# Performance work log

Measured on AMD Instinct MI355X. Metric: run time of the kernel, lower is better.

## Reference

```python
import jax, jax.numpy as jnp
import numpy as np

N_NODES = 100000
N_EDGES = 3200000
K_OPS = 6
D_FEAT = 64


def setup_inputs() -> dict:
    key = jax.random.key(0)
    k1, k2, k3, k4, k5 = jax.random.split(key, 5)
    h_ops = jax.random.normal(k1, (K_OPS, N_NODES, D_FEAT), dtype=jnp.float32)
    weights = jax.random.normal(k2, (K_OPS,), dtype=jnp.float32)  # mixed signs -> exercises w>0 skip
    vals = jax.random.uniform(k3, (N_EDGES,), dtype=jnp.float32)
    row = jnp.sort(jax.random.randint(k4, (N_EDGES,), 0, N_NODES, dtype=jnp.int32))
    col = jax.random.randint(k5, (N_EDGES,), 0, N_NODES, dtype=jnp.int32)
    return {"h_ops": h_ops, "weights": weights, "vals": vals, "row": row, "col": col}


def _spmm(row, col, vals, x, n):
    # sparse (n x n) COO @ dense (n x d): gather source rows, scale, scatter-add to dest rows
    msg = x[col] * vals[:, None]                                  # [E, d]
    return jax.ops.segment_sum(msg, row, num_segments=n, indices_are_sorted=True)


def reference(h_ops, weights, vals, row, col):
    # sum_k: (w_k * spmm(A, H_k)) if w_k > 0 else w_k (scalar broadcast)
    # spmm is linear, so positive-weight branch folds into one spmm of the weighted sum.
    n = h_ops.shape[1]
    pos = weights > 0
    w_pos = jnp.where(pos, weights, 0.0)                          # [K]
    combined = jnp.einsum("k,knd->nd", w_pos, h_ops)              # [N, d]
    out = _spmm(row, col, vals, combined, n)                      # [N, d]
    scalar_term = jnp.sum(jnp.where(pos, 0.0, weights))           # sum of skipped weights
    return out + scalar_term
```

## Files before the change

kernel.cpp:

```cpp
#include <hip/hip_runtime.h>

#define D_FEAT 64
#define MAX_K 8

__device__ __forceinline__ unsigned short f2bf_rne(float f) {
    unsigned int u = __float_as_uint(f);
    u += 0x7FFFu + ((u >> 16) & 1u);
    return (unsigned short)(u >> 16);
}

__device__ __forceinline__ float bf_lo(unsigned int d) { return __uint_as_float(d << 16); }
__device__ __forceinline__ float bf_hi(unsigned int d) { return __uint_as_float(d & 0xffff0000u); }

__global__ __launch_bounds__(256) void combine_bf16_kernel(
    const float* __restrict__ h_ops,
    const float* __restrict__ weights,
    unsigned short* __restrict__ combined,
    int total4, int K) {
    float w[MAX_K];
    for (int k = 0; k < K; ++k) {
        float wk = weights[k];
        w[k] = wk > 0.f ? wk : 0.f;
    }
    int stride = gridDim.x * blockDim.x;
    for (int i = blockIdx.x * blockDim.x + threadIdx.x; i < total4; i += stride) {
        float4 acc = make_float4(0.f, 0.f, 0.f, 0.f);
        for (int k = 0; k < K; ++k) {
            float4 v = reinterpret_cast<const float4*>(h_ops)[(size_t)k * total4 + i];
            acc.x = fmaf(w[k], v.x, acc.x);
            acc.y = fmaf(w[k], v.y, acc.y);
            acc.z = fmaf(w[k], v.z, acc.z);
            acc.w = fmaf(w[k], v.w, acc.w);
        }
        ushort4 o;
        o.x = f2bf_rne(acc.x); o.y = f2bf_rne(acc.y);
        o.z = f2bf_rne(acc.z); o.w = f2bf_rne(acc.w);
        reinterpret_cast<ushort4*>(combined)[i] = o;
    }
}

__global__ __launch_bounds__(256) void build_rowptr_kernel(
    const int* __restrict__ row, int* __restrict__ row_ptr, int E, int N) {
    int stride = gridDim.x * blockDim.x;
    for (int e = blockIdx.x * blockDim.x + threadIdx.x; e < E; e += stride) {
        int r = row[e];
        int rp = (e == 0) ? -1 : row[e - 1];
        for (int x = rp + 1; x <= r; ++x) row_ptr[x] = e;
        if (e == E - 1) {
            for (int x = r + 1; x <= N; ++x) row_ptr[x] = E;
        }
    }
}

__global__ __launch_bounds__(256) void spmm_bf16_w8_kernel(
    const unsigned short* __restrict__ combined,
    const float* __restrict__ vals,
    const int* __restrict__ row_ptr,
    const int* __restrict__ col,
    const float* __restrict__ weights,
    float* __restrict__ out,
    int n_nodes, int K) {
    int wid = (blockIdx.x * blockDim.x + threadIdx.x) >> 6;
    int lane = threadIdx.x & 63;
    if (wid >= n_nodes) return;

    float s = 0.f;
    for (int k = 0; k < K; ++k) {
        float wk = weights[k];
        if (!(wk > 0.f)) s += wk;
    }

    int start = row_ptr[wid];
    int end   = row_ptr[wid + 1];

    int sub = lane >> 3;
    int fl  = lane & 7;

    float a0 = 0.f, a1 = 0.f, a2 = 0.f, a3 = 0.f;
    float a4 = 0.f, a5 = 0.f, a6 = 0.f, a7 = 0.f;

    const uint4* cb = reinterpret_cast<const uint4*>(combined);

    for (int base = start; base < end; base += 16) {
        int iA = base + sub;
        int iB = base + 8 + sub;
        bool okA = iA < end;
        bool okB = iB < end;
        int iAc = okA ? iA : end - 1;
        int iBc = okB ? iB : end - 1;
        int cA = col[iAc];
        int cB = col[iBc];
        float vA = vals[iAc];
        float vB = vals[iBc];
        if (!okA) vA = 0.f;
        if (!okB) vB = 0.f;
        uint4 gA = cb[((size_t)cA << 3) + fl];
        uint4 gB = cb[((size_t)cB << 3) + fl];
        a0 = fmaf(vA, bf_lo(gA.x), a0); a1 = fmaf(vA, bf_hi(gA.x), a1);
        a2 = fmaf(vA, bf_lo(gA.y), a2); a3 = fmaf(vA, bf_hi(gA.y), a3);
        a4 = fmaf(vA, bf_lo(gA.z), a4); a5 = fmaf(vA, bf_hi(gA.z), a5);
        a6 = fmaf(vA, bf_lo(gA.w), a6); a7 = fmaf(vA, bf_hi(gA.w), a7);
        a0 = fmaf(vB, bf_lo(gB.x), a0); a1 = fmaf(vB, bf_hi(gB.x), a1);
        a2 = fmaf(vB, bf_lo(gB.y), a2); a3 = fmaf(vB, bf_hi(gB.y), a3);
        a4 = fmaf(vB, bf_lo(gB.z), a4); a5 = fmaf(vB, bf_hi(gB.z), a5);
        a6 = fmaf(vB, bf_lo(gB.w), a6); a7 = fmaf(vB, bf_hi(gB.w), a7);
    }

#pragma unroll
    for (int m = 8; m <= 32; m <<= 1) {
        a0 += __shfl_xor(a0, m, 64);
        a1 += __shfl_xor(a1, m, 64);
        a2 += __shfl_xor(a2, m, 64);
        a3 += __shfl_xor(a3, m, 64);
        a4 += __shfl_xor(a4, m, 64);
        a5 += __shfl_xor(a5, m, 64);
        a6 += __shfl_xor(a6, m, 64);
        a7 += __shfl_xor(a7, m, 64);
    }

    if (sub == 0) {
        float4* po = reinterpret_cast<float4*>(out + (size_t)wid * D_FEAT + fl * 8);
        po[0] = make_float4(a0 + s, a1 + s, a2 + s, a3 + s);
        po[1] = make_float4(a4 + s, a5 + s, a6 + s, a7 + s);
    }
}

__global__ __launch_bounds__(256) void combine_kernel(
    const float* __restrict__ h_ops,
    const float* __restrict__ weights,
    float* __restrict__ combined,
    int total4, int K) {
    float w[MAX_K];
    for (int k = 0; k < K; ++k) {
        float wk = weights[k];
        w[k] = wk > 0.f ? wk : 0.f;
    }
    int stride = gridDim.x * blockDim.x;
    for (int i = blockIdx.x * blockDim.x + threadIdx.x; i < total4; i += stride) {
        float4 acc = make_float4(0.f, 0.f, 0.f, 0.f);
        for (int k = 0; k < K; ++k) {
            float4 v = reinterpret_cast<const float4*>(h_ops)[(size_t)k * total4 + i];
            acc.x = fmaf(w[k], v.x, acc.x);
            acc.y = fmaf(w[k], v.y, acc.y);
            acc.z = fmaf(w[k], v.z, acc.z);
            acc.w = fmaf(w[k], v.w, acc.w);
        }
        reinterpret_cast<float4*>(combined)[i] = acc;
    }
}

__global__ __launch_bounds__(256) void spmm_kernel_bs(
    const float* __restrict__ combined,
    const float* __restrict__ vals,
    const int* __restrict__ row,
    const int* __restrict__ col,
    const float* __restrict__ weights,
    float* __restrict__ out,
    int n_nodes, int n_edges, int K) {
    int wid = (blockIdx.x * blockDim.x + threadIdx.x) >> 6;
    int lane = threadIdx.x & 63;
    if (wid >= n_nodes) return;

    int lo = 0, hi = n_edges;
    while (lo < hi) { int mid = (lo + hi) >> 1; if (row[mid] < wid) lo = mid + 1; else hi = mid; }
    int start = lo;
    hi = n_edges;
    while (lo < hi) { int mid = (lo + hi) >> 1; if (row[mid] <= wid) lo = mid + 1; else hi = mid; }
    int end = lo;

    float acc = 0.f;
    for (int e = start; e < end; ++e) {
        acc = fmaf(vals[e], combined[(size_t)col[e] * D_FEAT + lane], acc);
    }
    float s = 0.f;
    for (int k = 0; k < K; ++k) {
        float wk = weights[k];
        if (!(wk > 0.f)) s += wk;
    }
    out[(size_t)wid * D_FEAT + lane] = acc + s;
}

__global__ __launch_bounds__(256) void spmm_fused_kernel(
    const float* __restrict__ h_ops,
    const float* __restrict__ vals,
    const int* __restrict__ row,
    const int* __restrict__ col,
    const float* __restrict__ weights,
    float* __restrict__ out,
    int n_nodes, int n_edges, int K, size_t plane) {
    int wid = (blockIdx.x * blockDim.x + threadIdx.x) >> 6;
    int lane = threadIdx.x & 63;
    if (wid >= n_nodes) return;

    float w[MAX_K];
    for (int k = 0; k < K; ++k) {
        float wk = weights[k];
        w[k] = wk > 0.f ? wk : 0.f;
    }
    int lo = 0, hi = n_edges;
    while (lo < hi) { int mid = (lo + hi) >> 1; if (row[mid] < wid) lo = mid + 1; else hi = mid; }
    int start = lo;
    hi = n_edges;
    while (lo < hi) { int mid = (lo + hi) >> 1; if (row[mid] <= wid) lo = mid + 1; else hi = mid; }
    int end = lo;

    float acc = 0.f;
    for (int e = start; e < end; ++e) {
        int c = col[e];
        float v = vals[e];
        float comb = 0.f;
        for (int k = 0; k < K; ++k) {
            comb = fmaf(w[k], h_ops[(size_t)k * plane + (size_t)c * D_FEAT + lane], comb);
        }
        acc = fmaf(v, comb, acc);
    }
    float s = 0.f;
    for (int k = 0; k < K; ++k) {
        float wk = weights[k];
        if (!(wk > 0.f)) s += wk;
    }
    out[(size_t)wid * D_FEAT + lane] = acc + s;
}

extern "C" void kernel_launch(void* const* d_in, const int* in_sizes, int n_in,
                              void* d_out, int out_size, void* d_ws, size_t ws_size,
                              hipStream_t stream) {
    const float* h_ops   = (const float*)d_in[0];
    const float* weights = (const float*)d_in[1];
    const float* vals    = (const float*)d_in[2];
    const int*   row     = (const int*)d_in[3];
    const int*   col     = (const int*)d_in[4];
    float* out = (float*)d_out;

    int K = in_sizes[1];
    if (K > MAX_K) K = MAX_K;
    int E = in_sizes[2];
    int N = out_size / D_FEAT;
    int total = N * D_FEAT;
    size_t need_bf      = (size_t)total * sizeof(unsigned short);
    size_t need_rowptr  = (size_t)(N + 1) * sizeof(int);
    size_t need_f32     = (size_t)total * sizeof(float);

    int spmm_blocks = (N * 64 + 255) / 256;

    if (ws_size >= need_bf + need_rowptr) {
        unsigned short* combined = (unsigned short*)d_ws;
        int* row_ptr = (int*)((char*)d_ws + need_bf);
        int total4 = total / 4;
        combine_bf16_kernel<<<2048, 256, 0, stream>>>(h_ops, weights, combined, total4, K);
        build_rowptr_kernel<<<2048, 256, 0, stream>>>(row, row_ptr, E, N);
        spmm_bf16_w8_kernel<<<spmm_blocks, 256, 0, stream>>>(combined, vals, row_ptr, col,
                                                             weights, out, N, K);
    } else if (ws_size >= need_f32) {
        float* combined = (float*)d_ws;
        int total4 = total / 4;
        combine_kernel<<<2048, 256, 0, stream>>>(h_ops, weights, combined, total4, K);
        spmm_kernel_bs<<<spmm_blocks, 256, 0, stream>>>(combined, vals, row, col,
                                                        weights, out, N, E, K);
    } else {
        spmm_fused_kernel<<<spmm_blocks, 256, 0, stream>>>(h_ops, vals, row, col, weights,
                                                           out, N, E, K, (size_t)total);
    }
}
```

Before: 91.77 us.

## Merge combine and rowptr kernels, skip zero-weight ops, unroll SpMM edge loop

Merges the bf16 combine and row_ptr build kernels into one launch with block ranges split between the two tasks, removing a launch and letting both run concurrently. The combine loop now skips loading h_ops slices whose clamped weight is zero, cutting the HBM reads for non-positive weights. The SpMM inner loop handles 32 edges per iteration in four guarded groups instead of 16, giving more gathers in flight per wavefront. The branch on weights adds a little divergence-free control flow, and the extra edge groups raise register use.

After: 94.54 us. +3.0%, slower.

```diff
diff --git a/kernel.cpp b/kernel.cpp
--- a/kernel.cpp
+++ b/kernel.cpp
@@ -2,6 +2,8 @@
 
 #define D_FEAT 64
 #define MAX_K 8
+#define COMBINE_BLOCKS 2048
+#define ROWPTR_BLOCKS 512
 
 __device__ __forceinline__ unsigned short f2bf_rne(float f) {
     unsigned int u = __float_as_uint(f);
@@ -12,42 +14,45 @@
 __device__ __forceinline__ float bf_lo(unsigned int d) { return __uint_as_float(d << 16); }
 __device__ __forceinline__ float bf_hi(unsigned int d) { return __uint_as_float(d & 0xffff0000u); }
 
-__global__ __launch_bounds__(256) void combine_bf16_kernel(
+__global__ __launch_bounds__(256) void combine_rowptr_kernel(
     const float* __restrict__ h_ops,
     const float* __restrict__ weights,
     unsigned short* __restrict__ combined,
-    int total4, int K) {
-    float w[MAX_K];
-    for (int k = 0; k < K; ++k) {
-        float wk = weights[k];
-        w[k] = wk > 0.f ? wk : 0.f;
-    }
-    int stride = gridDim.x * blockDim.x;
-    for (int i = blockIdx.x * blockDim.x + threadIdx.x; i < total4; i += stride) {
-        float4 acc = make_float4(0.f, 0.f, 0.f, 0.f);
+    const int* __restrict__ row,
+    int* __restrict__ row_ptr,
+    int total4, int K, int E, int N) {
+    if (blockIdx.x < COMBINE_BLOCKS) {
+        float w[MAX_K];
         for (int k = 0; k < K; ++k) {
-            float4 v = reinterpret_cast<const float4*>(h_ops)[(size_t)k * total4 + i];
-            acc.x = fmaf(w[k], v.x, acc.x);
-            acc.y = fmaf(w[k], v.y, acc.y);
-            acc.z = fmaf(w[k], v.z, acc.z);
-            acc.w = fmaf(w[k], v.w, acc.w);
-        }
-        ushort4 o;
-        o.x = f2bf_rne(acc.x); o.y = f2bf_rne(acc.y);
-        o.z = f2bf_rne(acc.z); o.w = f2bf_rne(acc.w);
-        reinterpret_cast<ushort4*>(combined)[i] = o;
-    }
-}
-
-__global__ __launch_bounds__(256) void build_rowptr_kernel(
-    const int* __restrict__ row, int* __restrict__ row_ptr, int E, int N) {
-    int stride = gridDim.x * blockDim.x;
-    for (int e = blockIdx.x * blockDim.x + threadIdx.x; e < E; e += stride) {
-        int r = row[e];
-        int rp = (e == 0) ? -1 : row[e - 1];
-        for (int x = rp + 1; x <= r; ++x) row_ptr[x] = e;
-        if (e == E - 1) {
-            for (int x = r + 1; x <= N; ++x) row_ptr[x] = E;
+            float wk = weights[k];
+            w[k] = wk > 0.f ? wk : 0.f;
+        }
+        int stride = COMBINE_BLOCKS * 256;
+        for (int i = blockIdx.x * 256 + threadIdx.x; i < total4; i += stride) {
+            float4 acc = make_float4(0.f, 0.f, 0.f, 0.f);
+            for (int k = 0; k < K; ++k) {
+                if (w[k] != 0.f) {
+                    float4 v = reinterpret_cast<const float4*>(h_ops)[(size_t)k * total4 + i];
+                    acc.x = fmaf(w[k], v.x, acc.x);
+                    acc.y = fmaf(w[k], v.y, acc.y);
+                    acc.z = fmaf(w[k], v.z, acc.z);
+                    acc.w = fmaf(w[k], v.w, acc.w);
+                }
+            }
+            ushort4 o;
+            o.x = f2bf_rne(acc.x); o.y = f2bf_rne(acc.y);
+            o.z = f2bf_rne(acc.z); o.w = f2bf_rne(acc.w);
+            reinterpret_cast<ushort4*>(combined)[i] = o;
+        }
+    } else {
+        int stride = ROWPTR_BLOCKS * 256;
+        for (int e = (blockIdx.x - COMBINE_BLOCKS) * 256 + threadIdx.x; e < E; e += stride) {
+            int r = row[e];
+            int rp = (e == 0) ? -1 : row[e - 1];
+            for (int x = rp + 1; x <= r; ++x) row_ptr[x] = e;
+            if (e == E - 1) {
+                for (int x = r + 1; x <= N; ++x) row_ptr[x] = E;
+            }
         }
     }
 }
@@ -81,30 +86,27 @@
 
     const uint4* cb = reinterpret_cast<const uint4*>(combined);
 
-    for (int base = start; base < end; base += 16) {
-        int iA = base + sub;
-        int iB = base + 8 + sub;
-        bool okA = iA < end;
-        bool okB = iB < end;
-        int iAc = okA ? iA : end - 1;
-        int iBc = okB ? iB : end - 1;
-        int cA = col[iAc];
-        int cB = col[iBc];
-        float vA = vals[iAc];
-        float vB = vals[iBc];
-        if (!okA) vA = 0.f;
-        if (!okB) vB = 0.f;
-        uint4 gA = cb[((size_t)cA << 3) + fl];
-        uint4 gB = cb[((size_t)cB << 3) + fl];
-        a0 = fmaf(vA, bf_lo(gA.x), a0); a1 = fmaf(vA, bf_hi(gA.x), a1);
-        a2 = fmaf(vA, bf_lo(gA.y), a2); a3 = fmaf(vA, bf_hi(gA.y), a3);
-        a4 = fmaf(vA, bf_lo(gA.z), a4); a5 = fmaf(vA, bf_hi(gA.z), a5);
-        a6 = fmaf(vA, bf_lo(gA.w), a6); a7 = fmaf(vA, bf_hi(gA.w), a7);
-        a0 = fmaf(vB, bf_lo(gB.x), a0); a1 = fmaf(vB, bf_hi(gB.x), a1);
-        a2 = fmaf(vB, bf_lo(gB.y), a2); a3 = fmaf(vB, bf_hi(gB.y), a3);
-        a4 = fmaf(vB, bf_lo(gB.z), a4); a5 = fmaf(vB, bf_hi(gB.z), a5);
-        a6 = fmaf(vB, bf_lo(gB.w), a6); a7 = fmaf(vB, bf_hi(gB.w), a7);
-    }
+#define DO_GROUP(goff)                                                          \
+    {                                                                           \
+        int ii = base + (goff) + sub;                                           \
+        bool ok = ii < end;                                                     \
+        int ic = ok ? ii : end - 1;                                             \
+        int c = col[ic];                                                        \
+        float v = ok ? vals[ic] : 0.f;                                          \
+        uint4 g = cb[((size_t)c << 3) + fl];                                    \
+        a0 = fmaf(v, bf_lo(g.x), a0); a1 = fmaf(v, bf_hi(g.x), a1);             \
+        a2 = fmaf(v, bf_lo(g.y), a2); a3 = fmaf(v, bf_hi(g.y), a3);             \
+        a4 = fmaf(v, bf_lo(g.z), a4); a5 = fmaf(v, bf_hi(g.z), a5);             \
+        a6 = fmaf(v, bf_lo(g.w), a6); a7 = fmaf(v, bf_hi(g.w), a7);             \
+    }
+
+    for (int base = start; base < end; base += 32) {
+        DO_GROUP(0)
+        if (base + 8 < end)  DO_GROUP(8)
+        if (base + 16 < end) DO_GROUP(16)
+        if (base + 24 < end) DO_GROUP(24)
+    }
+#undef DO_GROUP
 
 #pragma unroll
     for (int m = 8; m <= 32; m <<= 1) {
@@ -139,11 +141,13 @@
     for (int i = blockIdx.x * blockDim.x + threadIdx.x; i < total4; i += stride) {
         float4 acc = make_float4(0.f, 0.f, 0.f, 0.f);
         for (int k = 0; k < K; ++k) {
-            float4 v = reinterpret_cast<const float4*>(h_ops)[(size_t)k * total4 + i];
-            acc.x = fmaf(w[k], v.x, acc.x);
-            acc.y = fmaf(w[k], v.y, acc.y);
-            acc.z = fmaf(w[k], v.z, acc.z);
-            acc.w = fmaf(w[k], v.w, acc.w);
+            if (w[k] != 0.f) {
+                float4 v = reinterpret_cast<const float4*>(h_ops)[(size_t)k * total4 + i];
+                acc.x = fmaf(w[k], v.x, acc.x);
+                acc.y = fmaf(w[k], v.y, acc.y);
+                acc.z = fmaf(w[k], v.z, acc.z);
+                acc.w = fmaf(w[k], v.w, acc.w);
+            }
         }
         reinterpret_cast<float4*>(combined)[i] = acc;
     }
@@ -247,8 +251,8 @@
         unsigned short* combined = (unsigned short*)d_ws;
         int* row_ptr = (int*)((char*)d_ws + need_bf);
         int total4 = total / 4;
-        combine_bf16_kernel<<<2048, 256, 0, stream>>>(h_ops, weights, combined, total4, K);
-        build_rowptr_kernel<<<2048, 256, 0, stream>>>(row, row_ptr, E, N);
+        combine_rowptr_kernel<<<COMBINE_BLOCKS + ROWPTR_BLOCKS, 256, 0, stream>>>(
+            h_ops, weights, combined, row, row_ptr, total4, K, E, N);
         spmm_bf16_w8_kernel<<<spmm_blocks, 256, 0, stream>>>(combined, vals, row_ptr, col,
                                                              weights, out, N, K);
     } else if (ws_size >= need_f32) {
```

## Fuse combine and row_ptr build into one launch, skip zero-weight operand loads

Applied to the files above, without the earlier changes.

Merges the weighted-combine and CSR row_ptr construction kernels into a single launch with block-range specialization, so the first 256 blocks build row_ptr while the rest combine. The combine path now fully unrolls over MAX_K, issues all loads up front, and skips loading h_ops slices whose clamped weight is zero, reducing HBM reads for non-positive weights. This removes one kernel launch and some memory traffic, but the row_ptr build gets fewer blocks and the register use per thread grows.

Measured after the change: 85.92 us. 6.4% less time.

```diff
diff --git a/kernel.cpp b/kernel.cpp
--- a/kernel.cpp
+++ b/kernel.cpp
@@ -2,6 +2,8 @@
 
 #define D_FEAT 64
 #define MAX_K 8
+#define ROWPTR_BLOCKS 256
+#define COMBINE_BLOCKS 2048
 
 __device__ __forceinline__ unsigned short f2bf_rne(float f) {
     unsigned int u = __float_as_uint(f);
@@ -12,42 +14,53 @@
 __device__ __forceinline__ float bf_lo(unsigned int d) { return __uint_as_float(d << 16); }
 __device__ __forceinline__ float bf_hi(unsigned int d) { return __uint_as_float(d & 0xffff0000u); }
 
-__global__ __launch_bounds__(256) void combine_bf16_kernel(
+__global__ __launch_bounds__(256) void combine_rowptr_kernel(
     const float* __restrict__ h_ops,
     const float* __restrict__ weights,
     unsigned short* __restrict__ combined,
-    int total4, int K) {
-    float w[MAX_K];
-    for (int k = 0; k < K; ++k) {
-        float wk = weights[k];
-        w[k] = wk > 0.f ? wk : 0.f;
-    }
-    int stride = gridDim.x * blockDim.x;
-    for (int i = blockIdx.x * blockDim.x + threadIdx.x; i < total4; i += stride) {
-        float4 acc = make_float4(0.f, 0.f, 0.f, 0.f);
-        for (int k = 0; k < K; ++k) {
-            float4 v = reinterpret_cast<const float4*>(h_ops)[(size_t)k * total4 + i];
-            acc.x = fmaf(w[k], v.x, acc.x);
-            acc.y = fmaf(w[k], v.y, acc.y);
-            acc.z = fmaf(w[k], v.z, acc.z);
-            acc.w = fmaf(w[k], v.w, acc.w);
-        }
-        ushort4 o;
-        o.x = f2bf_rne(acc.x); o.y = f2bf_rne(acc.y);
-        o.z = f2bf_rne(acc.z); o.w = f2bf_rne(acc.w);
-        reinterpret_cast<ushort4*>(combined)[i] = o;
-    }
-}
-
-__global__ __launch_bounds__(256) void build_rowptr_kernel(
-    const int* __restrict__ row, int* __restrict__ row_ptr, int E, int N) {
-    int stride = gridDim.x * blockDim.x;
-    for (int e = blockIdx.x * blockDim.x + threadIdx.x; e < E; e += stride) {
-        int r = row[e];
-        int rp = (e == 0) ? -1 : row[e - 1];
-        for (int x = rp + 1; x <= r; ++x) row_ptr[x] = e;
-        if (e == E - 1) {
-            for (int x = r + 1; x <= N; ++x) row_ptr[x] = E;
+    const int* __restrict__ row,
+    int* __restrict__ row_ptr,
+    int total4, int K, int E, int N) {
+    if (blockIdx.x < ROWPTR_BLOCKS) {
+        int stride = ROWPTR_BLOCKS * 256;
+        for (int e = blockIdx.x * 256 + threadIdx.x; e < E; e += stride) {
+            int r = row[e];
+            int rp = (e == 0) ? -1 : row[e - 1];
+            for (int x = rp + 1; x <= r; ++x) row_ptr[x] = e;
+            if (e == E - 1) {
+                for (int x = r + 1; x <= N; ++x) row_ptr[x] = E;
+            }
+        }
+    } else {
+        float w[MAX_K];
+#pragma unroll
+        for (int k = 0; k < MAX_K; ++k) {
+            float wk = (k < K) ? weights[k] : 0.f;
+            w[k] = wk > 0.f ? wk : 0.f;
+        }
+        int stride = COMBINE_BLOCKS * 256;
+        for (int i = (blockIdx.x - ROWPTR_BLOCKS) * 256 + threadIdx.x; i < total4; i += stride) {
+            float4 v[MAX_K];
+#pragma unroll
+            for (int k = 0; k < MAX_K; ++k) {
+                if (w[k] != 0.f) {
+                    v[k] = reinterpret_cast<const float4*>(h_ops)[(size_t)k * total4 + i];
+                }
+            }
+            float4 acc = make_float4(0.f, 0.f, 0.f, 0.f);
+#pragma unroll
+            for (int k = 0; k < MAX_K; ++k) {
+                if (w[k] != 0.f) {
+                    acc.x = fmaf(w[k], v[k].x, acc.x);
+                    acc.y = fmaf(w[k], v[k].y, acc.y);
+                    acc.z = fmaf(w[k], v[k].z, acc.z);
+                    acc.w = fmaf(w[k], v[k].w, acc.w);
+                }
+            }
+            ushort4 o;
+            o.x = f2bf_rne(acc.x); o.y = f2bf_rne(acc.y);
+            o.z = f2bf_rne(acc.z); o.w = f2bf_rne(acc.w);
+            reinterpret_cast<ushort4*>(combined)[i] = o;
         }
     }
 }
@@ -139,11 +152,13 @@
     for (int i = blockIdx.x * blockDim.x + threadIdx.x; i < total4; i += stride) {
         float4 acc = make_float4(0.f, 0.f, 0.f, 0.f);
         for (int k = 0; k < K; ++k) {
-            float4 v = reinterpret_cast<const float4*>(h_ops)[(size_t)k * total4 + i];
-            acc.x = fmaf(w[k], v.x, acc.x);
-            acc.y = fmaf(w[k], v.y, acc.y);
-            acc.z = fmaf(w[k], v.z, acc.z);
-            acc.w = fmaf(w[k], v.w, acc.w);
+            if (w[k] != 0.f) {
+                float4 v = reinterpret_cast<const float4*>(h_ops)[(size_t)k * total4 + i];
+                acc.x = fmaf(w[k], v.x, acc.x);
+                acc.y = fmaf(w[k], v.y, acc.y);
+                acc.z = fmaf(w[k], v.z, acc.z);
+                acc.w = fmaf(w[k], v.w, acc.w);
+            }
         }
         reinterpret_cast<float4*>(combined)[i] = acc;
     }
@@ -247,8 +262,8 @@
         unsigned short* combined = (unsigned short*)d_ws;
         int* row_ptr = (int*)((char*)d_ws + need_bf);
         int total4 = total / 4;
-        combine_bf16_kernel<<<2048, 256, 0, stream>>>(h_ops, weights, combined, total4, K);
-        build_rowptr_kernel<<<2048, 256, 0, stream>>>(row, row_ptr, E, N);
+        combine_rowptr_kernel<<<ROWPTR_BLOCKS + COMBINE_BLOCKS, 256, 0, stream>>>(
+            h_ops, weights, combined, row, row_ptr, total4, K, E, N);
         spmm_bf16_w8_kernel<<<spmm_blocks, 256, 0, stream>>>(combined, vals, row_ptr, col,
                                                              weights, out, N, K);
     } else if (ws_size >= need_f32) {
```
